# Kernel optimization log

Hardware: AMD Instinct MI355X
Metric: run time of the kernel (lower is better)

Reference implementation:

```python
import jax, jax.numpy as jnp
import numpy as np

NUM_STREAMS = 4
SINKHORN_ITERS = 10
TAU = 0.05


def sinkhorn_project(logits):
    # logits: [S, S] -> near doubly-stochastic matrix, log-domain Sinkhorn
    S = logits.shape[0]
    scaled = logits / TAU
    scaled = scaled - jnp.max(scaled)
    log_marginal = jnp.full((S,), -jnp.log(jnp.asarray(S, scaled.dtype)), dtype=scaled.dtype)
    u = jnp.zeros((S,), dtype=scaled.dtype)
    v = jnp.zeros((S,), dtype=scaled.dtype)

    def body(_, uv):
        u, v = uv
        u = log_marginal - jax.nn.logsumexp(scaled + v[None, :], axis=1)
        v = log_marginal - jax.nn.logsumexp(scaled + u[:, None], axis=0)
        return (u, v)

    u, v = jax.lax.fori_loop(0, SINKHORN_ITERS, body, (u, v))
    return jnp.exp(scaled + u[:, None] + v[None, :]) * S


def setup_inputs() -> dict:
    key = jax.random.key(0)
    k1, k2, k3, k4 = jax.random.split(key, 4)
    B_eff, T, D = 32, 2048, 1024  # B_eff = B * NUM_STREAMS
    streams = jax.random.normal(k1, (B_eff, T, D), dtype=jnp.float32)
    # params initialized like the module (base logit scale 8.0)
    base = 8.0
    h_res_logits = jnp.full((NUM_STREAMS, NUM_STREAMS), -base, dtype=jnp.float32)
    h_res_logits = h_res_logits.at[jnp.arange(NUM_STREAMS), jnp.arange(NUM_STREAMS)].set(0.0)
    h_res_logits = h_res_logits + 0.1 * jax.random.normal(k2, (NUM_STREAMS, NUM_STREAMS), dtype=jnp.float32)
    h_pre_logits = jnp.full((NUM_STREAMS,), -base, dtype=jnp.float32).at[0].set(0.0)
    h_pre_logits = h_pre_logits + 0.1 * jax.random.normal(k3, (NUM_STREAMS,), dtype=jnp.float32)
    h_post_logits = jnp.full((NUM_STREAMS,), -base, dtype=jnp.float32).at[0].set(0.0)
    h_post_logits = h_post_logits + 0.1 * jax.random.normal(k4, (NUM_STREAMS,), dtype=jnp.float32)
    return {"streams": streams, "h_res_logits": h_res_logits,
            "h_pre_logits": h_pre_logits, "h_post_logits": h_post_logits}


def reference(streams, h_res_logits, h_pre_logits, h_post_logits):
    S = NUM_STREAMS
    BS, T, D = streams.shape
    B = BS // S
    # [B*S, T, D] -> [B, T, S, D]
    x = streams.reshape(B, S, T, D).transpose(0, 2, 1, 3)
    h_res = sinkhorn_project(h_res_logits)           # [S, S]
    h_pre = jax.nn.softmax(h_pre_logits)             # [S]
    h_post = jax.nn.softmax(h_post_logits)           # [S]
    residual_mixed = jnp.einsum('ij,btjd->btid', h_res, x)   # [B, T, S, D]
    branch_input = jnp.einsum('s,btsd->btd', h_pre, x)       # [B, T, D]
    branch_output = branch_input  # branch_fn = identity
    out = residual_mixed + branch_output[:, :, None, :] * h_post[None, None, :, None]
    # [B, T, S, D] -> [B*S, T, D]
    return out.transpose(0, 2, 1, 3).reshape(B * S, T, D)
```

## Files before the change

### kernel.cpp

```cpp
#include <hip/hip_runtime.h>
#include <math.h>

#define NSTREAMS 4
#define SINKHORN_ITERS 10
#define TAU 0.05f
#define N4_SHIFT 19
#define TOTAL_ITEMS (8 << N4_SHIFT)

typedef float f32x4 __attribute__((ext_vector_type(4)));

__global__ void coeff_kernel(const float* __restrict__ res_logits,
                             const float* __restrict__ pre_logits,
                             const float* __restrict__ post_logits,
                             float* __restrict__ Mout) {
    if (threadIdx.x != 0 || blockIdx.x != 0) return;

    float scaled[NSTREAMS][NSTREAMS];
    float mx = -INFINITY;
    #pragma unroll
    for (int i = 0; i < NSTREAMS; ++i)
        #pragma unroll
        for (int j = 0; j < NSTREAMS; ++j) {
            float sv = res_logits[i * NSTREAMS + j] * (1.0f / TAU);
            scaled[i][j] = sv;
            mx = fmaxf(mx, sv);
        }
    #pragma unroll
    for (int i = 0; i < NSTREAMS; ++i)
        #pragma unroll
        for (int j = 0; j < NSTREAMS; ++j)
            scaled[i][j] -= mx;

    const float logm = -logf((float)NSTREAMS);
    float uu[NSTREAMS] = {0.f, 0.f, 0.f, 0.f};
    float vv[NSTREAMS] = {0.f, 0.f, 0.f, 0.f};

    for (int it = 0; it < SINKHORN_ITERS; ++it) {
        #pragma unroll
        for (int i = 0; i < NSTREAMS; ++i) {
            float m = -INFINITY;
            #pragma unroll
            for (int j = 0; j < NSTREAMS; ++j) m = fmaxf(m, scaled[i][j] + vv[j]);
            float s = 0.f;
            #pragma unroll
            for (int j = 0; j < NSTREAMS; ++j) s += expf(scaled[i][j] + vv[j] - m);
            uu[i] = logm - (m + logf(s));
        }
        #pragma unroll
        for (int j = 0; j < NSTREAMS; ++j) {
            float m = -INFINITY;
            #pragma unroll
            for (int i = 0; i < NSTREAMS; ++i) m = fmaxf(m, scaled[i][j] + uu[i]);
            float s = 0.f;
            #pragma unroll
            for (int i = 0; i < NSTREAMS; ++i) s += expf(scaled[i][j] + uu[i] - m);
            vv[j] = logm - (m + logf(s));
        }
    }

    float hres[NSTREAMS][NSTREAMS];
    #pragma unroll
    for (int i = 0; i < NSTREAMS; ++i)
        #pragma unroll
        for (int j = 0; j < NSTREAMS; ++j)
            hres[i][j] = expf(scaled[i][j] + uu[i] + vv[j]) * (float)NSTREAMS;

    float hpre[NSTREAMS], hpost[NSTREAMS];
    {
        float m = -INFINITY;
        #pragma unroll
        for (int k = 0; k < NSTREAMS; ++k) m = fmaxf(m, pre_logits[k]);
        float e[NSTREAMS], s = 0.f;
        #pragma unroll
        for (int k = 0; k < NSTREAMS; ++k) { e[k] = expf(pre_logits[k] - m); s += e[k]; }
        #pragma unroll
        for (int k = 0; k < NSTREAMS; ++k) hpre[k] = e[k] / s;
    }
    {
        float m = -INFINITY;
        #pragma unroll
        for (int k = 0; k < NSTREAMS; ++k) m = fmaxf(m, post_logits[k]);
        float e[NSTREAMS], s = 0.f;
        #pragma unroll
        for (int k = 0; k < NSTREAMS; ++k) { e[k] = expf(post_logits[k] - m); s += e[k]; }
        #pragma unroll
        for (int k = 0; k < NSTREAMS; ++k) hpost[k] = e[k] / s;
    }

    #pragma unroll
    for (int i = 0; i < NSTREAMS; ++i)
        #pragma unroll
        for (int j = 0; j < NSTREAMS; ++j)
            Mout[i * NSTREAMS + j] = hres[i][j] + hpost[i] * hpre[j];
}

__global__ __launch_bounds__(256) void mix_kernel(const f32x4* __restrict__ in,
                                                  f32x4* __restrict__ out,
                                                  const float* __restrict__ M) {
    float m[16];
    #pragma unroll
    for (int k = 0; k < 16; ++k) m[k] = M[k];

    const int p = blockIdx.x * 256 + threadIdx.x;
    const int b = p >> N4_SHIFT;
    const int r = p & ((1 << N4_SHIFT) - 1);
    const int base = (b << 2) << N4_SHIFT;

    const f32x4 x0 = in[base + (0 << N4_SHIFT) + r];
    const f32x4 x1 = in[base + (1 << N4_SHIFT) + r];
    const f32x4 x2 = in[base + (2 << N4_SHIFT) + r];
    const f32x4 x3 = in[base + (3 << N4_SHIFT) + r];

    #pragma unroll
    for (int i = 0; i < 4; ++i) {
        f32x4 o = m[i * 4 + 0] * x0;
        o += m[i * 4 + 1] * x1;
        o += m[i * 4 + 2] * x2;
        o += m[i * 4 + 3] * x3;
        out[base + (i << N4_SHIFT) + r] = o;
    }
}

extern "C" void kernel_launch(void* const* d_in, const int* in_sizes, int n_in,
                              void* d_out, int out_size, void* d_ws, size_t ws_size,
                              hipStream_t stream) {
    const float* streams     = (const float*)d_in[0];
    const float* h_res_log   = (const float*)d_in[1];
    const float* h_pre_log   = (const float*)d_in[2];
    const float* h_post_log  = (const float*)d_in[3];
    float* out = (float*)d_out;
    float* M   = (float*)d_ws;

    coeff_kernel<<<1, 64, 0, stream>>>(h_res_log, h_pre_log, h_post_log, M);

    mix_kernel<<<TOTAL_ITEMS / 256, 256, 0, stream>>>(
        (const f32x4*)streams, (f32x4*)out, M);
}
```

Baseline: 460.1 us.

## Stage stream tiles in LDS so each wave handles one output stream

Each block now loads a 1024-element (float4) chunk from all four streams into shared memory. Each wave reads and writes a contiguous run for a single stream, and the mixing weights for that wave's output row are read after a barrier. The goal is longer contiguous per-wave memory streams and fewer outstanding-load registers per thread, with 4096 blocks each doing 16 items per thread. In exchange it adds 64KB of LDS per block, which limits occupancy, plus a block-wide barrier between load and compute that can stall memory overlap.

```diff
diff --git a/kernel.cpp b/kernel.cpp
--- a/kernel.cpp
+++ b/kernel.cpp
@@ -5,7 +5,6 @@
 #define SINKHORN_ITERS 10
 #define TAU 0.05f
 #define N4_SHIFT 19
-#define TOTAL_ITEMS (8 << N4_SHIFT)
 
 typedef float f32x4 __attribute__((ext_vector_type(4)));
 
@@ -97,27 +96,38 @@
 __global__ __launch_bounds__(256) void mix_kernel(const f32x4* __restrict__ in,
                                                   f32x4* __restrict__ out,
                                                   const float* __restrict__ M) {
-    float m[16];
+    __shared__ f32x4 lds[4][1024];
+
+    const int bid   = blockIdx.x;
+    const int b     = bid >> 9;
+    const int chunk = bid & 511;
+    const int r0    = chunk << 10;
+    const int w     = threadIdx.x >> 6;
+    const int l     = threadIdx.x & 63;
+    const int base  = (b << 2) << N4_SHIFT;
+
+    const f32x4* src = in + base + (w << N4_SHIFT) + r0;
     #pragma unroll
-    for (int k = 0; k < 16; ++k) m[k] = M[k];
+    for (int k = 0; k < 16; ++k) {
+        const int item = (k << 6) + l;
+        lds[w][item] = src[item];
+    }
+    __syncthreads();
 
-    const int p = blockIdx.x * 256 + threadIdx.x;
-    const int b = p >> N4_SHIFT;
-    const int r = p & ((1 << N4_SHIFT) - 1);
-    const int base = (b << 2) << N4_SHIFT;
+    const float m0 = M[w * 4 + 0];
+    const float m1 = M[w * 4 + 1];
+    const float m2 = M[w * 4 + 2];
+    const float m3 = M[w * 4 + 3];
 
-    const f32x4 x0 = in[base + (0 << N4_SHIFT) + r];
-    const f32x4 x1 = in[base + (1 << N4_SHIFT) + r];
-    const f32x4 x2 = in[base + (2 << N4_SHIFT) + r];
-    const f32x4 x3 = in[base + (3 << N4_SHIFT) + r];
-
+    f32x4* dst = out + base + (w << N4_SHIFT) + r0;
     #pragma unroll
-    for (int i = 0; i < 4; ++i) {
-        f32x4 o = m[i * 4 + 0] * x0;
-        o += m[i * 4 + 1] * x1;
-        o += m[i * 4 + 2] * x2;
-        o += m[i * 4 + 3] * x3;
-        out[base + (i << N4_SHIFT) + r] = o;
+    for (int k = 0; k < 16; ++k) {
+        const int item = (k << 6) + l;
+        f32x4 o = m0 * lds[0][item];
+        o += m1 * lds[1][item];
+        o += m2 * lds[2][item];
+        o += m3 * lds[3][item];
+        dst[item] = o;
     }
 }
 
@@ -133,6 +143,5 @@
 
     coeff_kernel<<<1, 64, 0, stream>>>(h_res_log, h_pre_log, h_post_log, M);
 
-    mix_kernel<<<TOTAL_ITEMS / 256, 256, 0, stream>>>(
-        (const f32x4*)streams, (f32x4*)out, M);
+    mix_kernel<<<4096, 256, 0, stream>>>((const f32x4*)streams, (f32x4*)out, M);
 }
```

After: 464.1 us. Within noise of the previous version (+0.9%).
